# Kernel optimization log

Measured on AMD Instinct MI355X. Metric: run time of the kernel, lower is better.

The kernel has to match this reference:

```python
import jax, jax.numpy as jnp
import numpy as np

LEVEL_N = [81920, 20480, 5120, 1280, 320]  # faces at div..div-4 (div=6, 20*4^d)
K = 10  # SpherePHD conv kernel taps
W_SHAPES = [(64,3),(64,64),(128,64),(128,128),(256,128),(256,256),(256,256),(512,256),(512,512),(512,512),(512,512),(512,512),(512,512)]
BLOCKS = [[0,1],[2,3],[4,5,6],[7,8,9],[10,11,12]]  # conv indices per VGG block


def setup_inputs() -> dict:
    key = jax.random.key(0)
    ks = iter(jax.random.split(key, 64))
    d = {"x": jax.random.normal(next(ks), (2, 3, LEVEL_N[0]), jnp.float32)}
    for l, n in enumerate(LEVEL_N):
        d[f"conv_t{l}"] = jax.random.randint(next(ks), (n, K), 0, n, jnp.int32)
        d[f"adj_t{l}"] = jax.random.randint(next(ks), (n, 4), 0, n, jnp.int32)
        d[f"pool_t{l}"] = jax.random.randint(next(ks), (n // 4,), 0, n, jnp.int32)
    for i, (o, c) in enumerate(W_SHAPES):
        d[f"w{i}"] = jax.random.normal(next(ks), (o, c, K), jnp.float32) * (1.0 / np.sqrt(c * K))
        d[f"b{i}"] = jnp.zeros((o,), jnp.float32)
    return d


def phd_conv(x, w, b, table):
    # x: [B,C,N], table: [N,K] -> gather neighbors [B,C,N,K], weighted sum, ReLU
    g = x[:, :, table]
    y = jnp.einsum('bcnk,ock->bon', g, w) + b[None, :, None]
    return jax.nn.relu(y)


def phd_maxpool(x, adj, pool):
    # max over adjacent faces, then subsample to parent faces
    m = jnp.max(x[:, :, adj], axis=-1)  # [B,C,N]
    return m[:, :, pool]                # [B,C,N/4]


def reference(x, conv_t0, conv_t1, conv_t2, conv_t3, conv_t4,
              adj_t0, adj_t1, adj_t2, adj_t3, adj_t4,
              pool_t0, pool_t1, pool_t2, pool_t3, pool_t4,
              w0, w1, w2, w3, w4, w5, w6, w7, w8, w9, w10, w11, w12,
              b0, b1, b2, b3, b4, b5, b6, b7, b8, b9, b10, b11, b12):
    conv_ts = [conv_t0, conv_t1, conv_t2, conv_t3, conv_t4]
    adj_ts = [adj_t0, adj_t1, adj_t2, adj_t3, adj_t4]
    pool_ts = [pool_t0, pool_t1, pool_t2, pool_t3, pool_t4]
    ws = [w0, w1, w2, w3, w4, w5, w6, w7, w8, w9, w10, w11, w12]
    bs = [b0, b1, b2, b3, b4, b5, b6, b7, b8, b9, b10, b11, b12]
    h = x
    for lvl, idxs in enumerate(BLOCKS):
        for i in idxs:
            h = phd_conv(h, ws[i], bs[i], conv_ts[lvl])
        h = phd_maxpool(h, adj_ts[lvl], pool_ts[lvl])
    return h  # [2, 512, 80]
```

## Files before the change

### kernel.cpp

```cpp
#include <hip/hip_runtime.h>
#include <stdint.h>

typedef __bf16 bf16;
typedef bf16 bf16x8 __attribute__((ext_vector_type(8)));
typedef float f32x4 __attribute__((ext_vector_type(4)));
typedef unsigned short u16x8 __attribute__((ext_vector_type(8)));

__device__ __forceinline__ void gload_lds16(const bf16* g, bf16* l) {
    __builtin_amdgcn_global_load_lds(
        (const __attribute__((address_space(1))) void*)g,
        (__attribute__((address_space(3))) void*)l, 16, 0, 0);
}

template<int C>
__device__ __forceinline__ void cvt_pair(const float* __restrict__ src,
                                         bf16* __restrict__ dst,
                                         int tp, int base5)
{
    int ocp = tp - base5;
    int oc  = ocp * 2;
    int o   = oc / C;
    int c   = oc & (C - 1);
    const f32x4* s4 = (const f32x4*)(src + (size_t)oc * 10);
    float v[20];
#pragma unroll
    for (int j = 0; j < 5; j++) {
        f32x4 p = s4[j];
#pragma unroll
        for (int e = 0; e < 4; e++) v[4 * j + e] = p[e];
    }
    unsigned short* d = (unsigned short*)(dst + (size_t)base5 * 20
                                              + (size_t)o * 10 * C + c);
#pragma unroll
    for (int k = 0; k < 10; k++) {
        union { bf16 h; unsigned short u; } a, b;
        a.h = (bf16)v[k];
        b.h = (bf16)v[10 + k];
        uint32_t pk = (uint32_t)a.u | ((uint32_t)b.u << 16);
        *(uint32_t*)(d + (size_t)k * C) = pk;
    }
}

__global__ __launch_bounds__(256) void prep_w(
    const float* w1, const float* w2, const float* w3, const float* w4,
    const float* w5, const float* w6, const float* w7, const float* w8,
    const float* w9, const float* w10, const float* w11, const float* w12,
    bf16* __restrict__ dst)
{
    int t = blockIdx.x * 256 + threadIdx.x;
    if (t >= 817152) return;
    if      (t <   2048) cvt_pair< 64>(w1,  dst, t, 0);
    else if (t <   6144) cvt_pair< 64>(w2,  dst, t, 2048);
    else if (t <  14336) cvt_pair<128>(w3,  dst, t, 6144);
    else if (t <  30720) cvt_pair<128>(w4,  dst, t, 14336);
    else if (t <  63488) cvt_pair<256>(w5,  dst, t, 30720);
    else if (t <  96256) cvt_pair<256>(w6,  dst, t, 63488);
    else if (t < 161792) cvt_pair<256>(w7,  dst, t, 96256);
    else if (t < 292864) cvt_pair<512>(w8,  dst, t, 161792);
    else if (t < 423936) cvt_pair<512>(w9,  dst, t, 292864);
    else if (t < 555008) cvt_pair<512>(w10, dst, t, 423936);
    else if (t < 686080) cvt_pair<512>(w11, dst, t, 555008);
    else                 cvt_pair<512>(w12, dst, t, 686080);
}

__global__ __launch_bounds__(256) void conv0_kernel(
    const float* __restrict__ x, const float* __restrict__ w0,
    const float* __restrict__ b0, const int* __restrict__ table,
    bf16* __restrict__ out)
{
    const int N = 81920;
    __shared__ float wls[30][64];
    __shared__ float bls[64];
    int tid = threadIdx.x;
    for (int i = tid; i < 1920; i += 256) {
        int o = i / 30, ck = i - o * 30;
        wls[ck][o] = w0[i];
    }
    if (tid < 64) bls[tid] = b0[tid];
    __syncthreads();

    int p = blockIdx.x * 256 + tid;
    int b = p >= N;
    int n = p - b * N;
    int idx[10];
    const int* trow = table + n * 10;
#pragma unroll
    for (int k = 0; k < 10; k++) idx[k] = trow[k];
    float xv[30];
#pragma unroll
    for (int c = 0; c < 3; c++)
#pragma unroll
        for (int k = 0; k < 10; k++)
            xv[c * 10 + k] = x[(b * 3 + c) * N + idx[k]];

    float acc[64];
#pragma unroll
    for (int o = 0; o < 64; o++) acc[o] = bls[o];
    for (int ck = 0; ck < 30; ck++) {
        float xs = xv[ck];
        const f32x4* wrow = (const f32x4*)(&wls[ck][0]);
#pragma unroll
        for (int o4 = 0; o4 < 16; o4++) {
            f32x4 w4 = wrow[o4];
            acc[o4 * 4 + 0] += xs * w4[0];
            acc[o4 * 4 + 1] += xs * w4[1];
            acc[o4 * 4 + 2] += xs * w4[2];
            acc[o4 * 4 + 3] += xs * w4[3];
        }
    }
    bf16x8 ob[8];
#pragma unroll
    for (int i = 0; i < 8; i++)
#pragma unroll
        for (int e = 0; e < 8; e++)
            ob[i][e] = (bf16)fmaxf(acc[i * 8 + e], 0.0f);
    bf16x8* dst = (bf16x8*)(out + (size_t)p * 64);
#pragma unroll
    for (int i = 0; i < 8; i++) dst[i] = ob[i];
}

__global__ __launch_bounds__(256, 1) void conv_reg64(
    const bf16* __restrict__ in, const bf16* __restrict__ w,
    const float* __restrict__ bias, const int* __restrict__ table,
    bf16* __restrict__ out, int N)
{
    __shared__ bf16 Ws[10][64][64];

    const int tid = threadIdx.x;
    const int lane = tid & 63;
    const int wid = tid >> 6;
    const int l16 = lane & 15, q = lane >> 4;
    const int sx = l16 & 7;

    {
        int lrow8 = lane >> 3;
        int lseg  = lane & 7;
#pragma unroll
        for (int t = 0; t < 20; t++) {
            int u = wid * 20 + t;
            int k = u >> 3;
            int rb = u & 7;
            int row = rb * 8 + lrow8;
            int gs = lseg ^ (row & 7);
            gload_lds16(w + (size_t)row * 640 + k * 64 + gs * 8,
                        &Ws[k][rb * 8][0]);
        }
    }

    const int p0 = blockIdx.x * 128 + wid * 32;

    int nrow[2][10];
#pragma unroll
    for (int tp = 0; tp < 2; tp++) {
        int p = p0 + tp * 16 + l16;
        int b = p >= N;
        int n = p - b * N;
        const int* tr = table + n * 10;
#pragma unroll
        for (int k = 0; k < 10; k++)
            nrow[tp][k] = (b * N + tr[k]) * 64;
    }
    const bf16* xq = in + q * 8;

    f32x4 acc[4][2];
#pragma unroll
    for (int a = 0; a < 4; a++)
#pragma unroll
        for (int c = 0; c < 2; c++) acc[a][c] = (f32x4){0.f, 0.f, 0.f, 0.f};

    auto loadX = [&](int k, bf16x8 (&B)[2][2]) {
#pragma unroll
        for (int tp = 0; tp < 2; tp++)
#pragma unroll
            for (int ks = 0; ks < 2; ks++)
                B[tp][ks] = *(const bf16x8*)(xq + nrow[tp][k] + ks * 32);
    };
    auto mmc = [&](int k, bf16x8 (&B)[2][2]) {
#pragma unroll
        for (int ks = 0; ks < 2; ks++) {
            bf16x8 af[4];
#pragma unroll
            for (int to = 0; to < 4; to++) {
                int row = to * 16 + l16;
                int s = (ks * 4 + q) ^ sx;
                af[to] = *(const bf16x8*)(&Ws[k][row][s * 8]);
            }
#pragma unroll
            for (int to = 0; to < 4; to++)
#pragma unroll
                for (int tp = 0; tp < 2; tp++)
                    acc[to][tp] = __builtin_amdgcn_mfma_f32_16x16x32_bf16(
                        af[to], B[tp][ks], acc[to][tp], 0, 0, 0);
        }
    };

    bf16x8 B0[2][2], B1[2][2], B2[2][2], B3[2][2];
    loadX(0, B0); loadX(1, B1); loadX(2, B2); loadX(3, B3);

    asm volatile("s_waitcnt vmcnt(16)" ::: "memory");
    __builtin_amdgcn_s_barrier();

    mmc(0, B0); loadX(4, B0);
    mmc(1, B1); loadX(5, B1);
    mmc(2, B2); loadX(6, B2);
    mmc(3, B3); loadX(7, B3);
    mmc(4, B0); loadX(8, B0);
    mmc(5, B1); loadX(9, B1);
    mmc(6, B2);
    mmc(7, B3);
    mmc(8, B0);
    mmc(9, B1);

#pragma unroll
    for (int to = 0; to < 4; ++to) {
        int ob = to * 16 + q * 4;
        f32x4 bv = *(const f32x4*)(bias + ob);
#pragma unroll
        for (int tp = 0; tp < 2; ++tp) {
            int p = p0 + tp * 16 + l16;
            union { ushort4 u4; unsigned short s[4]; } pk;
#pragma unroll
            for (int r = 0; r < 4; r++) {
                float v = fmaxf(acc[to][tp][r] + bv[r], 0.0f);
                union { bf16 h; unsigned short u; } cc;
                cc.h = (bf16)v;
                pk.s[r] = cc.u;
            }
            *(ushort4*)(out + (size_t)p * 64 + ob) = pk.u4;
        }
    }
}

template<int C, int BP, int BO, int WO, int WP>
__global__ __launch_bounds__(256) void conv_p(
    const bf16* __restrict__ in, const bf16* __restrict__ w,
    const float* __restrict__ bias, const int* __restrict__ table,
    bf16* __restrict__ out, float* __restrict__ slab,
    int N, int O, int S, int PO)
{
    constexpr int CH = C / 64;
    constexpr int CHUNKS = CH * 10;
    constexpr int CK = C * 10;
    constexpr int TO = (BO / WO) / 16;
    constexpr int TP = (BP / WP) / 16;
    constexpr int XI = BP / 32;
    constexpr int WI = BO / 32;
    constexpr int LPS = XI + WI;
    static_assert(LPS == 4, "vmcnt literal assumes 4 loads/stage");

    __shared__ bf16 Xs[4][BP][64];
    __shared__ bf16 Ws[4][BO][64];
    __shared__ int rowoff[BP][10];

    const int tid = threadIdx.x;
    const int lane = tid & 63;
    const int wid = tid >> 6;
    const int wo = wid & (WO - 1), wp = wid / WO;
    const int l16 = lane & 15, q = lane >> 4;

    const int p0 = blockIdx.x * BP;
    const int o0 = blockIdx.y * BO;
    const int z = blockIdx.z;

    for (int j = tid; j < BP * 10; j += 256) {
        int pp = j / 10, k = j - pp * 10;
        int p = p0 + pp;
        int b = p >= N;
        int n = p - b * N;
        rowoff[pp][k] = (b * N + table[n * 10 + k]) * C;
    }
    __syncthreads();

    int xsrow[XI], xgseg[XI];
#pragma unroll
    for (int t = 0; t < XI; t++) {
        int row = wid * (BP / 4) + t * 8 + (lane >> 3);
        xsrow[t] = row;
        xgseg[t] = (lane & 7) ^ (row & 7);
    }
    const bf16* wbase[WI];
#pragma unroll
    for (int t = 0; t < WI; t++) {
        int row = wid * (BO / 4) + t * 8 + (lane >> 3);
        int gs = (lane & 7) ^ (row & 7);
        wbase[t] = w + (size_t)(o0 + row) * CK + gs * 8;
    }

    const int per = CHUNKS / S;
    const int c0chunk = z * per;

    auto stage = [&](int chunk, int b4) {
        int k = chunk / CH;
        int cofs = (chunk & (CH - 1)) * 64;
#pragma unroll
        for (int t = 0; t < XI; t++) {
            int ro = rowoff[xsrow[t]][k];
            gload_lds16(in + ro + cofs + xgseg[t] * 8,
                        &Xs[b4][wid * (BP / 4) + t * 8][0]);
        }
#pragma unroll
        for (int t = 0; t < WI; t++)
            gload_lds16(wbase[t] + chunk * 64,
                        &Ws[b4][wid * (BO / 4) + t * 8][0]);
    };

    f32x4 acc[TO][TP];
#pragma unroll
    for (int a = 0; a < TO; a++)
#pragma unroll
        for (int c = 0; c < TP; c++) acc[a][c] = (f32x4){0.f, 0.f, 0.f, 0.f};

    stage(c0chunk, 0);
    stage(c0chunk + 1, 1);
    stage(c0chunk + 2, 2);

    const int obase = wo * (BO / WO);
    const int pbase = wp * (BP / WP);
    const int arow = obase + l16;
    const int brow = pbase + l16;
    const int sx = l16 & 7;

    for (int i = 0; i < per; i++) {
        const int bi = i & 3;
        asm volatile("s_waitcnt vmcnt(8)" ::: "memory");
        __builtin_amdgcn_s_barrier();
        const bf16* xb = &Xs[bi][0][0];
        const bf16* wb = &Ws[bi][0][0];
#pragma unroll
        for (int ks = 0; ks < 2; ks++) {
            int slot = ((ks * 4 + q) ^ sx) * 8;
            bf16x8 af[TO], bfr[TP];
#pragma unroll
            for (int to = 0; to < TO; to++)
                af[to] = *(const bf16x8*)(wb + (arow + to * 16) * 64 + slot);
#pragma unroll
            for (int tp = 0; tp < TP; tp++)
                bfr[tp] = *(const bf16x8*)(xb + (brow + tp * 16) * 64 + slot);
#pragma unroll
            for (int to = 0; to < TO; to++)
#pragma unroll
                for (int tp = 0; tp < TP; tp++)
                    acc[to][tp] = __builtin_amdgcn_mfma_f32_16x16x32_bf16(
                        af[to], bfr[tp], acc[to][tp], 0, 0, 0);
        }
        int nx = i + 3 < per ? i + 3 : per - 1;
        stage(c0chunk + nx, nx & 3);
    }

    if (S == 1) {
#pragma unroll
        for (int to = 0; to < TO; ++to) {
            int ob = o0 + obase + to * 16 + q * 4;
            f32x4 bv = *(const f32x4*)(bias + ob);
#pragma unroll
            for (int tp = 0; tp < TP; ++tp) {
                int p = p0 + pbase + tp * 16 + l16;
                union { ushort4 u4; unsigned short s[4]; } pk;
#pragma unroll
                for (int r = 0; r < 4; r++) {
                    float v = fmaxf(acc[to][tp][r] + bv[r], 0.0f);
                    union { bf16 h; unsigned short u; } cc;
                    cc.h = (bf16)v;
                    pk.s[r] = cc.u;
                }
                *(ushort4*)(out + (size_t)p * O + ob) = pk.u4;
            }
        }
    } else {
        float* sb = slab + (size_t)z * PO;
#pragma unroll
        for (int to = 0; to < TO; ++to) {
            int ob = o0 + obase + to * 16 + q * 4;
#pragma unroll
            for (int tp = 0; tp < TP; ++tp) {
                int p = p0 + pbase + tp * 16 + l16;
                *(f32x4*)(sb + (size_t)p * O + ob) = acc[to][tp];
            }
        }
    }
}

__global__ __launch_bounds__(256) void epi_reduce(
    const float* __restrict__ slab, const float* __restrict__ bias,
    bf16* __restrict__ out, int PO, int Omask, int S)
{
    int t4 = (blockIdx.x * 256 + threadIdx.x) * 4;
    if (t4 >= PO) return;
    f32x4 s = *(const f32x4*)(slab + t4);
    for (int zz = 1; zz < S; zz++)
        s += *(const f32x4*)(slab + (size_t)zz * PO + t4);
    int o = t4 & Omask;
    f32x4 bv = *(const f32x4*)(bias + o);
    union { ushort4 u4; unsigned short e[4]; } pk;
#pragma unroll
    for (int r = 0; r < 4; r++) {
        float v = fmaxf(s[r] + bv[r], 0.0f);
        union { bf16 h; unsigned short u; } cc;
        cc.h = (bf16)v;
        pk.e[r] = cc.u;
    }
    *(ushort4*)((unsigned short*)out + t4) = pk.u4;
}

__global__ __launch_bounds__(256) void pool_kernel(
    const bf16* __restrict__ in, const int* __restrict__ adj,
    const int* __restrict__ pool, bf16* __restrict__ out,
    int N, int M, int c8shift)
{
    int t = blockIdx.x * 256 + threadIdx.x;
    int total = M << c8shift;
    if (t >= total) return;
    int cc = t & ((1 << c8shift) - 1);
    int j = t >> c8shift;
    int b = blockIdx.y;
    int C = 8 << c8shift;
    int s = pool[j];
    const int* a = adj + s * 4;
    const unsigned short* inu = (const unsigned short*)in;
    size_t base = (size_t)b * N * C + (size_t)cc * 8;
    u16x8 m = *(const u16x8*)(inu + base + (size_t)a[0] * C);
#pragma unroll
    for (int i = 1; i < 4; i++) {
        u16x8 v = *(const u16x8*)(inu + base + (size_t)a[i] * C);
#pragma unroll
        for (int e = 0; e < 8; e++) m[e] = v[e] > m[e] ? v[e] : m[e];
    }
    *(u16x8*)((unsigned short*)out + ((size_t)b * M + j) * C + (size_t)cc * 8) = m;
}

__global__ __launch_bounds__(256) void final_pool(
    const bf16* __restrict__ in, const int* __restrict__ adj,
    const int* __restrict__ pool, float* __restrict__ out)
{
    int t = blockIdx.x * 256 + threadIdx.x;
    if (t >= 81920) return;
    int j = t % 80;
    int rest = t / 80;
    int c = rest & 511;
    int b = rest >> 9;
    int s = pool[j];
    const int* a = adj + s * 4;
    float m = 0.0f;
#pragma unroll
    for (int i = 0; i < 4; i++) {
        float v = (float)in[((size_t)b * 320 + a[i]) * 512 + c];
        m = fmaxf(m, v);
    }
    out[t] = m;
}

extern "C" void kernel_launch(void* const* d_in, const int* in_sizes, int n_in,
                              void* d_out, int out_size, void* d_ws, size_t ws_size,
                              hipStream_t stream)
{
    const float* x = (const float*)d_in[0];
    const int* convT[5]; const int* adjT[5]; const int* poolT[5];
    for (int l = 0; l < 5; l++) {
        convT[l] = (const int*)d_in[1 + 3 * l];
        adjT[l]  = (const int*)d_in[2 + 3 * l];
        poolT[l] = (const int*)d_in[3 + 3 * l];
    }
    const float* W[13]; const float* Bs[13];
    for (int i = 0; i < 13; i++) {
        W[i]  = (const float*)d_in[16 + 2 * i];
        Bs[i] = (const float*)d_in[17 + 2 * i];
    }

    bf16* wbf   = (bf16*)d_ws;
    bf16* A     = (bf16*)((char*)d_ws + (40u << 20));
    bf16* Bb    = (bf16*)((char*)d_ws + (70u << 20));
    float* slabA = (float*)((char*)d_ws + (100u << 20));
    float* slabB = (float*)((char*)d_ws + (130u << 20));

    static const int woff[13] = {0, 0, 40960, 122880, 286720, 614400, 1269760,
                                 1925120, 3235840, 5857280, 8478720, 11100160, 13721600};

    prep_w<<<dim3(817152 / 256), dim3(256), 0, stream>>>(
        W[1], W[2], W[3], W[4], W[5], W[6], W[7], W[8], W[9], W[10], W[11], W[12], wbf);

    conv0_kernel<<<dim3(640), dim3(256), 0, stream>>>(x, W[0], Bs[0], convT[0], A);

    const int PO3 = 2560 * 512;
    const int PO4 = 640 * 512;

    conv_reg64<<<dim3(1280), dim3(256), 0, stream>>>(
        A, wbf + woff[1], Bs[1], convT[0], Bb, 81920);
    pool_kernel<<<dim3(640, 2), dim3(256), 0, stream>>>(Bb, adjT[0], poolT[0], A, 81920, 20480, 3);
    conv_p<64, 64, 64, 2, 2><<<dim3(640, 2, 1), dim3(256), 0, stream>>>(
        A, wbf + woff[2], Bs[2], convT[1], Bb, nullptr, 20480, 128, 1, 0);
    conv_p<128, 64, 64, 2, 2><<<dim3(640, 2, 1), dim3(256), 0, stream>>>(
        Bb, wbf + woff[3], Bs[3], convT[1], A, nullptr, 20480, 128, 1, 0);
    pool_kernel<<<dim3(320, 2), dim3(256), 0, stream>>>(A, adjT[1], poolT[1], Bb, 20480, 5120, 4);
    conv_p<128, 64, 64, 2, 2><<<dim3(160, 4, 1), dim3(256), 0, stream>>>(
        Bb, wbf + woff[4], Bs[4], convT[2], A, nullptr, 5120, 256, 1, 0);
    conv_p<256, 64, 64, 2, 2><<<dim3(160, 4, 1), dim3(256), 0, stream>>>(
        A, wbf + woff[5], Bs[5], convT[2], Bb, nullptr, 5120, 256, 1, 0);
    conv_p<256, 64, 64, 2, 2><<<dim3(160, 4, 1), dim3(256), 0, stream>>>(
        Bb, wbf + woff[6], Bs[6], convT[2], A, nullptr, 5120, 256, 1, 0);
    pool_kernel<<<dim3(160, 2), dim3(256), 0, stream>>>(A, adjT[2], poolT[2], Bb, 5120, 1280, 5);
    conv_p<256, 64, 64, 2, 2><<<dim3(40, 8, 2), dim3(256), 0, stream>>>(
        Bb, wbf + woff[7], Bs[7], convT[3], nullptr, slabA, 1280, 512, 2, PO3);
    epi_reduce<<<dim3(PO3 / 1024), dim3(256), 0, stream>>>(slabA, Bs[7], A, PO3, 511, 2);
    conv_p<512, 64, 64, 2, 2><<<dim3(40, 8, 2), dim3(256), 0, stream>>>(
        A, wbf + woff[8], Bs[8], convT[3], nullptr, slabB, 1280, 512, 2, PO3);
    epi_reduce<<<dim3(PO3 / 1024), dim3(256), 0, stream>>>(slabB, Bs[8], Bb, PO3, 511, 2);
    conv_p<512, 64, 64, 2, 2><<<dim3(40, 8, 2), dim3(256), 0, stream>>>(
        Bb, wbf + woff[9], Bs[9], convT[3], nullptr, slabA, 1280, 512, 2, PO3);
    epi_reduce<<<dim3(PO3 / 1024), dim3(256), 0, stream>>>(slabA, Bs[9], A, PO3, 511, 2);
    pool_kernel<<<dim3(80, 2), dim3(256), 0, stream>>>(A, adjT[3], poolT[3], Bb, 1280, 320, 6);
    conv_p<512, 64, 64, 2, 2><<<dim3(10, 8, 8), dim3(256), 0, stream>>>(
        Bb, wbf + woff[10], Bs[10], convT[4], nullptr, slabA, 320, 512, 8, PO4);
    epi_reduce<<<dim3(PO4 / 1024), dim3(256), 0, stream>>>(slabA, Bs[10], A, PO4, 511, 8);
    conv_p<512, 64, 64, 2, 2><<<dim3(10, 8, 8), dim3(256), 0, stream>>>(
        A, wbf + woff[11], Bs[11], convT[4], nullptr, slabB, 320, 512, 8, PO4);
    epi_reduce<<<dim3(PO4 / 1024), dim3(256), 0, stream>>>(slabB, Bs[11], Bb, PO4, 511, 8);
    conv_p<512, 64, 64, 2, 2><<<dim3(10, 8, 8), dim3(256), 0, stream>>>(
        Bb, wbf + woff[12], Bs[12], convT[4], nullptr, slabA, 320, 512, 8, PO4);
    epi_reduce<<<dim3(PO4 / 1024), dim3(256), 0, stream>>>(slabA, Bs[12], A, PO4, 511, 8);

    final_pool<<<dim3(320), dim3(256), 0, stream>>>(A, adjT[4], poolT[4], (float*)d_out);
}
```

Before: 621.5 us.

## Replace LDS-staged gather conv with direct register loads and software pipelining

The conv kernel no longer stages gathered activations and weights through shared memory with a 4-deep async buffer and barriers. Each lane now loads its MFMA operands straight from global memory into registers: weights double-buffered, gathered neighbour rows four-deep, in an unrolled rotation over 10-chunk groups. Launch bounds request 2 blocks per CU. This removes LDS traffic and block barriers, but every wave now fetches its own operands, with no sharing between waves. It also raises register pressure and issues many uncoalesced 16-byte global loads.

```diff
diff --git a/kernel.cpp b/kernel.cpp
--- a/kernel.cpp
+++ b/kernel.cpp
@@ -231,8 +231,8 @@
     }
 }
 
-template<int C, int BP, int BO, int WO, int WP>
-__global__ __launch_bounds__(256) void conv_p(
+template<int C>
+__global__ __launch_bounds__(256, 2) void conv_rd(
     const bf16* __restrict__ in, const bf16* __restrict__ w,
     const float* __restrict__ bias, const int* __restrict__ table,
     bf16* __restrict__ out, float* __restrict__ slab,
@@ -241,120 +241,103 @@
     constexpr int CH = C / 64;
     constexpr int CHUNKS = CH * 10;
     constexpr int CK = C * 10;
-    constexpr int TO = (BO / WO) / 16;
-    constexpr int TP = (BP / WP) / 16;
-    constexpr int XI = BP / 32;
-    constexpr int WI = BO / 32;
-    constexpr int LPS = XI + WI;
-    static_assert(LPS == 4, "vmcnt literal assumes 4 loads/stage");
-
-    __shared__ bf16 Xs[4][BP][64];
-    __shared__ bf16 Ws[4][BO][64];
-    __shared__ int rowoff[BP][10];
 
     const int tid = threadIdx.x;
     const int lane = tid & 63;
     const int wid = tid >> 6;
-    const int wo = wid & (WO - 1), wp = wid / WO;
+    const int wo = wid & 1, wp = wid >> 1;
     const int l16 = lane & 15, q = lane >> 4;
 
-    const int p0 = blockIdx.x * BP;
-    const int o0 = blockIdx.y * BO;
+    const int p0 = blockIdx.x * 64;
+    const int o0 = blockIdx.y * 64;
     const int z = blockIdx.z;
-
-    for (int j = tid; j < BP * 10; j += 256) {
-        int pp = j / 10, k = j - pp * 10;
-        int p = p0 + pp;
+    const int per = CHUNKS / S;
+    const int c0 = z * per;
+    const int cend = c0 + per;
+
+    int nrow[2][10];
+#pragma unroll
+    for (int tp = 0; tp < 2; tp++) {
+        int p = p0 + wp * 32 + tp * 16 + l16;
         int b = p >= N;
         int n = p - b * N;
-        rowoff[pp][k] = (b * N + table[n * 10 + k]) * C;
-    }
-    __syncthreads();
-
-    int xsrow[XI], xgseg[XI];
-#pragma unroll
-    for (int t = 0; t < XI; t++) {
-        int row = wid * (BP / 4) + t * 8 + (lane >> 3);
-        xsrow[t] = row;
-        xgseg[t] = (lane & 7) ^ (row & 7);
-    }
-    const bf16* wbase[WI];
-#pragma unroll
-    for (int t = 0; t < WI; t++) {
-        int row = wid * (BO / 4) + t * 8 + (lane >> 3);
-        int gs = (lane & 7) ^ (row & 7);
-        wbase[t] = w + (size_t)(o0 + row) * CK + gs * 8;
-    }
-
-    const int per = CHUNKS / S;
-    const int c0chunk = z * per;
-
-    auto stage = [&](int chunk, int b4) {
-        int k = chunk / CH;
-        int cofs = (chunk & (CH - 1)) * 64;
-#pragma unroll
-        for (int t = 0; t < XI; t++) {
-            int ro = rowoff[xsrow[t]][k];
-            gload_lds16(in + ro + cofs + xgseg[t] * 8,
-                        &Xs[b4][wid * (BP / 4) + t * 8][0]);
-        }
-#pragma unroll
-        for (int t = 0; t < WI; t++)
-            gload_lds16(wbase[t] + chunk * 64,
-                        &Ws[b4][wid * (BO / 4) + t * 8][0]);
+        const int* tr = table + n * 10;
+#pragma unroll
+        for (int k = 0; k < 10; k++)
+            nrow[tp][k] = (b * N + tr[k]) * C;
+    }
+    const bf16* xq = in + q * 8;
+    const bf16* wb0 = w + (size_t)(o0 + wo * 32 + l16) * CK + q * 8;
+    const bf16* wb1 = wb0 + (size_t)16 * CK;
+
+    f32x4 acc[2][2];
+#pragma unroll
+    for (int a = 0; a < 2; a++)
+#pragma unroll
+        for (int c = 0; c < 2; c++) acc[a][c] = (f32x4){0.f, 0.f, 0.f, 0.f};
+
+    auto clampg = [&](int g) { return g < cend ? g : cend - 1; };
+
+    auto loadA = [&](int g, bf16x8 (&A)[2][2]) {
+        A[0][0] = *(const bf16x8*)(wb0 + g * 64);
+        A[0][1] = *(const bf16x8*)(wb0 + g * 64 + 32);
+        A[1][0] = *(const bf16x8*)(wb1 + g * 64);
+        A[1][1] = *(const bf16x8*)(wb1 + g * 64 + 32);
     };
-
-    f32x4 acc[TO][TP];
-#pragma unroll
-    for (int a = 0; a < TO; a++)
-#pragma unroll
-        for (int c = 0; c < TP; c++) acc[a][c] = (f32x4){0.f, 0.f, 0.f, 0.f};
-
-    stage(c0chunk, 0);
-    stage(c0chunk + 1, 1);
-    stage(c0chunk + 2, 2);
-
-    const int obase = wo * (BO / WO);
-    const int pbase = wp * (BP / WP);
-    const int arow = obase + l16;
-    const int brow = pbase + l16;
-    const int sx = l16 & 7;
-
-    for (int i = 0; i < per; i++) {
-        const int bi = i & 3;
-        asm volatile("s_waitcnt vmcnt(8)" ::: "memory");
-        __builtin_amdgcn_s_barrier();
-        const bf16* xb = &Xs[bi][0][0];
-        const bf16* wb = &Ws[bi][0][0];
-#pragma unroll
-        for (int ks = 0; ks < 2; ks++) {
-            int slot = ((ks * 4 + q) ^ sx) * 8;
-            bf16x8 af[TO], bfr[TP];
-#pragma unroll
-            for (int to = 0; to < TO; to++)
-                af[to] = *(const bf16x8*)(wb + (arow + to * 16) * 64 + slot);
-#pragma unroll
-            for (int tp = 0; tp < TP; tp++)
-                bfr[tp] = *(const bf16x8*)(xb + (brow + tp * 16) * 64 + slot);
-#pragma unroll
-            for (int to = 0; to < TO; to++)
-#pragma unroll
-                for (int tp = 0; tp < TP; tp++)
+    auto loadX = [&](int g, bf16x8 (&B)[2][2]) {
+        int k = g / CH;
+        int cofs = (g & (CH - 1)) * 64;
+#pragma unroll
+        for (int tp = 0; tp < 2; tp++)
+#pragma unroll
+            for (int ks = 0; ks < 2; ks++)
+                B[tp][ks] = *(const bf16x8*)(xq + nrow[tp][k] + cofs + ks * 32);
+    };
+    auto mmc = [&](bf16x8 (&A)[2][2], bf16x8 (&B)[2][2]) {
+#pragma unroll
+        for (int ks = 0; ks < 2; ks++)
+#pragma unroll
+            for (int to = 0; to < 2; to++)
+#pragma unroll
+                for (int tp = 0; tp < 2; tp++)
                     acc[to][tp] = __builtin_amdgcn_mfma_f32_16x16x32_bf16(
-                        af[to], bfr[tp], acc[to][tp], 0, 0, 0);
-        }
-        int nx = i + 3 < per ? i + 3 : per - 1;
-        stage(c0chunk + nx, nx & 3);
+                        A[to][ks], B[tp][ks], acc[to][tp], 0, 0, 0);
+    };
+
+    bf16x8 A0[2][2], A1[2][2];
+    bf16x8 B0[2][2], B1[2][2], B2[2][2], B3[2][2];
+
+    loadA(c0, A0); loadA(clampg(c0 + 1), A1);
+    loadX(c0, B0); loadX(clampg(c0 + 1), B1);
+    loadX(clampg(c0 + 2), B2); loadX(clampg(c0 + 3), B3);
+
+    auto body10 = [&](int g, bf16x8 (&Ba)[2][2], bf16x8 (&Bb)[2][2],
+                      bf16x8 (&Bc)[2][2], bf16x8 (&Bd)[2][2]) {
+        mmc(A0, Ba); loadA(clampg(g + 2), A0); loadX(clampg(g + 4),  Ba);
+        mmc(A1, Bb); loadA(clampg(g + 3), A1); loadX(clampg(g + 5),  Bb);
+        mmc(A0, Bc); loadA(clampg(g + 4), A0); loadX(clampg(g + 6),  Bc);
+        mmc(A1, Bd); loadA(clampg(g + 5), A1); loadX(clampg(g + 7),  Bd);
+        mmc(A0, Ba); loadA(clampg(g + 6), A0); loadX(clampg(g + 8),  Ba);
+        mmc(A1, Bb); loadA(clampg(g + 7), A1); loadX(clampg(g + 9),  Bb);
+        mmc(A0, Bc); loadA(clampg(g + 8), A0); loadX(clampg(g + 10), Bc);
+        mmc(A1, Bd); loadA(clampg(g + 9), A1); loadX(clampg(g + 11), Bd);
+        mmc(A0, Ba); loadA(clampg(g + 10), A0); loadX(clampg(g + 12), Ba);
+        mmc(A1, Bb); loadA(clampg(g + 11), A1); loadX(clampg(g + 13), Bb);
+    };
+
+    for (int t = 0; t < per; t += 20) {
+        body10(c0 + t, B0, B1, B2, B3);
+        if (t + 10 < per) body10(c0 + t + 10, B2, B3, B0, B1);
     }
 
     if (S == 1) {
 #pragma unroll
-        for (int to = 0; to < TO; ++to) {
-            int ob = o0 + obase + to * 16 + q * 4;
+        for (int to = 0; to < 2; ++to) {
+            int ob = o0 + wo * 32 + to * 16 + q * 4;
             f32x4 bv = *(const f32x4*)(bias + ob);
 #pragma unroll
-            for (int tp = 0; tp < TP; ++tp) {
-                int p = p0 + pbase + tp * 16 + l16;
+            for (int tp = 0; tp < 2; ++tp) {
+                int p = p0 + wp * 32 + tp * 16 + l16;
                 union { ushort4 u4; unsigned short s[4]; } pk;
 #pragma unroll
                 for (int r = 0; r < 4; r++) {
@@ -369,11 +352,11 @@
     } else {
         float* sb = slab + (size_t)z * PO;
 #pragma unroll
-        for (int to = 0; to < TO; ++to) {
-            int ob = o0 + obase + to * 16 + q * 4;
-#pragma unroll
-            for (int tp = 0; tp < TP; ++tp) {
-                int p = p0 + pbase + tp * 16 + l16;
+        for (int to = 0; to < 2; ++to) {
+            int ob = o0 + wo * 32 + to * 16 + q * 4;
+#pragma unroll
+            for (int tp = 0; tp < 2; ++tp) {
+                int p = p0 + wp * 32 + tp * 16 + l16;
                 *(f32x4*)(sb + (size_t)p * O + ob) = acc[to][tp];
             }
         }
@@ -486,35 +469,35 @@
     conv_reg64<<<dim3(1280), dim3(256), 0, stream>>>(
         A, wbf + woff[1], Bs[1], convT[0], Bb, 81920);
     pool_kernel<<<dim3(640, 2), dim3(256), 0, stream>>>(Bb, adjT[0], poolT[0], A, 81920, 20480, 3);
-    conv_p<64, 64, 64, 2, 2><<<dim3(640, 2, 1), dim3(256), 0, stream>>>(
+    conv_rd<64><<<dim3(640, 2, 1), dim3(256), 0, stream>>>(
         A, wbf + woff[2], Bs[2], convT[1], Bb, nullptr, 20480, 128, 1, 0);
-    conv_p<128, 64, 64, 2, 2><<<dim3(640, 2, 1), dim3(256), 0, stream>>>(
+    conv_rd<128><<<dim3(640, 2, 1), dim3(256), 0, stream>>>(
         Bb, wbf + woff[3], Bs[3], convT[1], A, nullptr, 20480, 128, 1, 0);
     pool_kernel<<<dim3(320, 2), dim3(256), 0, stream>>>(A, adjT[1], poolT[1], Bb, 20480, 5120, 4);
-    conv_p<128, 64, 64, 2, 2><<<dim3(160, 4, 1), dim3(256), 0, stream>>>(
+    conv_rd<128><<<dim3(160, 4, 1), dim3(256), 0, stream>>>(
         Bb, wbf + woff[4], Bs[4], convT[2], A, nullptr, 5120, 256, 1, 0);
-    conv_p<256, 64, 64, 2, 2><<<dim3(160, 4, 1), dim3(256), 0, stream>>>(
+    conv_rd<256><<<dim3(160, 4, 1), dim3(256), 0, stream>>>(
         A, wbf + woff[5], Bs[5], convT[2], Bb, nullptr, 5120, 256, 1, 0);
-    conv_p<256, 64, 64, 2, 2><<<dim3(160, 4, 1), dim3(256), 0, stream>>>(
+    conv_rd<256><<<dim3(160, 4, 1), dim3(256), 0, stream>>>(
         Bb, wbf + woff[6], Bs[6], convT[2], A, nullptr, 5120, 256, 1, 0);
     pool_kernel<<<dim3(160, 2), dim3(256), 0, stream>>>(A, adjT[2], poolT[2], Bb, 5120, 1280, 5);
-    conv_p<256, 64, 64, 2, 2><<<dim3(40, 8, 2), dim3(256), 0, stream>>>(
+    conv_rd<256><<<dim3(40, 8, 2), dim3(256), 0, stream>>>(
         Bb, wbf + woff[7], Bs[7], convT[3], nullptr, slabA, 1280, 512, 2, PO3);
     epi_reduce<<<dim3(PO3 / 1024), dim3(256), 0, stream>>>(slabA, Bs[7], A, PO3, 511, 2);
-    conv_p<512, 64, 64, 2, 2><<<dim3(40, 8, 2), dim3(256), 0, stream>>>(
+    conv_rd<512><<<dim3(40, 8, 2), dim3(256), 0, stream>>>(
         A, wbf + woff[8], Bs[8], convT[3], nullptr, slabB, 1280, 512, 2, PO3);
     epi_reduce<<<dim3(PO3 / 1024), dim3(256), 0, stream>>>(slabB, Bs[8], Bb, PO3, 511, 2);
-    conv_p<512, 64, 64, 2, 2><<<dim3(40, 8, 2), dim3(256), 0, stream>>>(
+    conv_rd<512><<<dim3(40, 8, 2), dim3(256), 0, stream>>>(
         Bb, wbf + woff[9], Bs[9], convT[3], nullptr, slabA, 1280, 512, 2, PO3);
     epi_reduce<<<dim3(PO3 / 1024), dim3(256), 0, stream>>>(slabA, Bs[9], A, PO3, 511, 2);
     pool_kernel<<<dim3(80, 2), dim3(256), 0, stream>>>(A, adjT[3], poolT[3], Bb, 1280, 320, 6);
-    conv_p<512, 64, 64, 2, 2><<<dim3(10, 8, 8), dim3(256), 0, stream>>>(
+    conv_rd<512><<<dim3(10, 8, 8), dim3(256), 0, stream>>>(
         Bb, wbf + woff[10], Bs[10], convT[4], nullptr, slabA, 320, 512, 8, PO4);
     epi_reduce<<<dim3(PO4 / 1024), dim3(256), 0, stream>>>(slabA, Bs[10], A, PO4, 511, 8);
-    conv_p<512, 64, 64, 2, 2><<<dim3(10, 8, 8), dim3(256), 0, stream>>>(
+    conv_rd<512><<<dim3(10, 8, 8), dim3(256), 0, stream>>>(
         A, wbf + woff[11], Bs[11], convT[4], nullptr, slabB, 320, 512, 8, PO4);
     epi_reduce<<<dim3(PO4 / 1024), dim3(256), 0, stream>>>(slabB, Bs[11], Bb, PO4, 511, 8);
-    conv_p<512, 64, 64, 2, 2><<<dim3(10, 8, 8), dim3(256), 0, stream>>>(
+    conv_rd<512><<<dim3(10, 8, 8), dim3(256), 0, stream>>>(
         Bb, wbf + woff[12], Bs[12], convT[4], nullptr, slabA, 320, 512, 8, PO4);
     epi_reduce<<<dim3(PO4 / 1024), dim3(256), 0, stream>>>(slabA, Bs[12], A, PO4, 511, 8);
 
```

New measurement: 1.135 ms. 82.7% more time.
